# Optimization experiments

Measured on AMD Instinct MI355X. Metric: run time of the kernel, lower is better.

## Reference

```python
import jax, jax.numpy as jnp
import numpy as np

D_MODEL, D_STATE, D_CONV, EXPAND = 1024, 16, 4, 2
D_INNER = EXPAND * D_MODEL
B, L = 2, 2048


def setup_inputs() -> dict:
    key = jax.random.key(0)
    ks = jax.random.split(key, 8)
    s = lambda fan: 1.0 / np.sqrt(fan)
    x = jax.random.normal(ks[0], (B, L, D_MODEL), dtype=jnp.float32)
    W_in = jax.random.normal(ks[1], (2 * D_INNER, D_MODEL), dtype=jnp.float32) * s(D_MODEL)
    conv_w = jax.random.normal(ks[2], (D_INNER, 1, D_CONV), dtype=jnp.float32) * s(D_CONV)
    conv_b = jax.random.normal(ks[3], (D_INNER,), dtype=jnp.float32) * 0.01
    A_log = jnp.log(jnp.abs(jax.random.normal(ks[4], (D_INNER, D_STATE), dtype=jnp.float32)) + 1e-4)
    Dp = jnp.ones((D_INNER,), dtype=jnp.float32)
    W_dt = jax.random.normal(ks[5], (D_INNER, D_INNER), dtype=jnp.float32) * s(D_INNER)
    b_dt = jax.random.normal(ks[6], (D_INNER,), dtype=jnp.float32) * 0.01
    W_out = jax.random.normal(ks[7], (D_MODEL, D_INNER), dtype=jnp.float32) * s(D_INNER)
    return {"x": x, "W_in": W_in, "conv_w": conv_w, "conv_b": conv_b,
            "A_log": A_log, "Dp": Dp, "W_dt": W_dt, "b_dt": b_dt, "W_out": W_out}


def _mamba_fwd(x, W_in, conv_w, conv_b, A_log, Dp, W_dt, b_dt, W_out):
    Bsz, Ln, _ = x.shape
    xz = x @ W_in.T                                  # [B, L, 2*d_inner]
    x_proj, z = jnp.split(xz, 2, axis=-1)            # each [B, L, d_inner]
    # depthwise causal conv1d: left-pad d_conv-1 (matches torch pad + [:L] slice)
    xc = jnp.transpose(x_proj, (0, 2, 1))            # [B, C, L]
    xc = jax.lax.conv_general_dilated(
        xc, conv_w, window_strides=(1,), padding=[(D_CONV - 1, 0)],
        dimension_numbers=("NCH", "OIH", "NCH"), feature_group_count=D_INNER)
    xc = xc + conv_b[None, :, None]
    x_act = jax.nn.silu(jnp.transpose(xc, (0, 2, 1)))  # [B, L, d_inner]
    dt = jax.nn.softplus(x_act @ W_dt.T + b_dt)        # [B, L, d_inner]
    A = -jnp.exp(A_log)                                # [d_inner, d_state]

    def step(h, inp):
        xt, dt_t = inp                                 # [B, d_inner] each
        dA = jnp.exp(dt_t[:, :, None] * A[None])       # [B, d_inner, d_state]
        dB = (dt_t * xt)[:, :, None]                   # broadcast over states
        h = dA * h + dB
        y_t = h.sum(axis=-1) + Dp * xt                 # [B, d_inner]
        return h, y_t

    h0 = jnp.zeros((Bsz, D_INNER, D_STATE), dtype=x.dtype)
    xs = (jnp.transpose(x_act, (1, 0, 2)), jnp.transpose(dt, (1, 0, 2)))  # [L, B, d_inner]
    _, ys = jax.lax.scan(step, h0, xs)
    y_ssm = jnp.transpose(ys, (1, 0, 2))               # [B, L, d_inner]
    y_gated = y_ssm * jax.nn.silu(z)
    return y_gated @ W_out.T                           # [B, L, d_model]


def reference(x, W_in, conv_w, conv_b, A_log, Dp, W_dt, b_dt, W_out):
    return _mamba_fwd(x, W_in, conv_w, conv_b, A_log, Dp, W_dt, b_dt, W_out)
```

## Files before the change

### kernel.cpp

```cpp
#include <hip/hip_runtime.h>

#define DMODEL 1024
#define DSTATE 16
#define DCONV  4
#define DINNER 2048
#define BSZ    2
#define LSEQ   2048
#define MTOT   (BSZ * LSEQ)
#define NCH    64
#define LC     (LSEQ / NCH)
#define LOG2E  1.44269504088896f

typedef unsigned short u16;
typedef __attribute__((ext_vector_type(8))) short short8;
typedef __attribute__((ext_vector_type(8))) unsigned short u16x8;
typedef __attribute__((ext_vector_type(4))) float f32x4;

__device__ __forceinline__ float silu_f(float v) {
  return v * __builtin_amdgcn_rcpf(1.f + __builtin_amdgcn_exp2f(-v * LOG2E));
}

__device__ __forceinline__ u16 f2bf(float f) {
  unsigned int u = __float_as_uint(f);
  u += 0x7FFF + ((u >> 16) & 1);
  return (u16)(u >> 16);
}
__device__ __forceinline__ float bf2f(u16 b) { return __uint_as_float(((unsigned int)b) << 16); }

__device__ __forceinline__ void gload_lds16(const u16* g, u16* l) {
  __builtin_amdgcn_global_load_lds((const __attribute__((address_space(1))) unsigned int*)g,
                                   (__attribute__((address_space(3))) unsigned int*)l, 16, 0, 0);
}

__global__ __launch_bounds__(256)
void cast4(const float4* __restrict__ s0, ushort4* __restrict__ d0, int n0,
           const float4* __restrict__ s1, ushort4* __restrict__ d1, int n1,
           const float4* __restrict__ s2, ushort4* __restrict__ d2, int n2,
           const float4* __restrict__ s3, ushort4* __restrict__ d3, int n3) {
  int i = blockIdx.x * 256 + threadIdx.x;
  const float4* s; ushort4* d;
  if (i < n0)                { s = s0; d = d0; }
  else if ((i -= n0) < n1)   { s = s1; d = d1; }
  else if ((i -= n1) < n2)   { s = s2; d = d2; }
  else if ((i -= n2) < n3)   { s = s3; d = d3; }
  else return;
  float4 v = s[i];
  ushort4 o = { f2bf(v.x), f2bf(v.y), f2bf(v.z), f2bf(v.w) };
  d[i] = o;
}

template<int MODE, int OBF>
__global__ __launch_bounds__(256)
void hgemm64(const u16* __restrict__ A, const u16* __restrict__ B,
             const float* __restrict__ bias, void* __restrict__ Cv,
             int M, int N, int K) {
  __shared__ u16 As[128 * 64];
  __shared__ u16 Bs[128 * 64];
  const int tid  = threadIdx.x;
  const int lane = tid & 63;
  const int w    = tid >> 6;
  const int quad = lane >> 4;
  const int l16  = lane & 15;

  const int nbn = N >> 7, nbm = M >> 7;
  const int pid = blockIdx.x;
  const int npg = 4 * nbn;
  const int fm  = (pid / npg) * 4;
  const int gsz = (nbm - fm < 4) ? (nbm - fm) : 4;
  const int bm  = (fm + (pid % gsz)) << 7;
  const int bn  = ((pid % npg) / gsz) << 7;

  const int wm = (w & 1) * 64;
  const int wn = (w >> 1) * 64;

  const int rseg = lane >> 3;
  const int cd   = (lane & 7) ^ rseg;
  const u16* Ag[4]; const u16* Bg[4]; u16* Al[4]; u16* Bl[4];
#pragma unroll
  for (int s = 0; s < 4; ++s) {
    const int sg = w * 4 + s;
    const int r  = sg * 8 + rseg;
    Ag[s] = A + (size_t)(bm + r) * K + (cd << 3);
    Bg[s] = B + (size_t)(bn + r) * K + (cd << 3);
    Al[s] = &As[sg << 9];
    Bl[s] = &Bs[sg << 9];
  }

  const short8* Afp[4][2];
  const short8* Bfp[4][2];
#pragma unroll
  for (int t = 0; t < 4; ++t) {
    const int ra = wm + 16 * t + l16;
    const int rb = wn + 16 * t + l16;
#pragma unroll
    for (int ks = 0; ks < 2; ++ks) {
      Afp[t][ks] = (const short8*)&As[ra * 64 + (((quad + 4 * ks) ^ (ra & 7)) << 3)];
      Bfp[t][ks] = (const short8*)&Bs[rb * 64 + (((quad + 4 * ks) ^ (rb & 7)) << 3)];
    }
  }

  f32x4 acc[4][4] = {};

  for (int k0 = 0; k0 < K; k0 += 64) {
#pragma unroll
    for (int s = 0; s < 4; ++s) {
      gload_lds16(Ag[s], Al[s]);
      gload_lds16(Bg[s], Bl[s]);
      Ag[s] += 64; Bg[s] += 64;
    }
    __syncthreads();
#pragma unroll
    for (int ks = 0; ks < 2; ++ks) {
      short8 af[4], bf[4];
#pragma unroll
      for (int t = 0; t < 4; ++t) { af[t] = *Afp[t][ks]; bf[t] = *Bfp[t][ks]; }
#pragma unroll
      for (int ti = 0; ti < 4; ++ti)
#pragma unroll
        for (int tj = 0; tj < 4; ++tj)
          acc[ti][tj] = __builtin_amdgcn_mfma_f32_16x16x32_bf16(af[ti], bf[tj],
                                                                acc[ti][tj], 0, 0, 0);
    }
    __syncthreads();
  }

#pragma unroll
  for (int ti = 0; ti < 4; ++ti) {
    const int row0 = bm + wm + 16 * ti + quad * 4;
#pragma unroll
    for (int tj = 0; tj < 4; ++tj) {
      const int col = bn + wn + 16 * tj + l16;
      const float bv = (MODE == 1) ? bias[col] : 0.f;
#pragma unroll
      for (int i = 0; i < 4; ++i) {
        float v = acc[ti][tj][i] + bv;
        if (MODE == 1) v = (v > 20.f) ? v : __logf(1.f + __expf(v));
        if (OBF) ((u16*)Cv)[(size_t)(row0 + i) * N + col] = f2bf(v);
        else     ((float*)Cv)[(size_t)(row0 + i) * N + col] = v;
      }
    }
  }
}

__global__ __launch_bounds__(256)
void conv_silu(const u16* __restrict__ xz, const float* __restrict__ conv_w,
               const float* __restrict__ conv_b, u16* __restrict__ xact) {
  const int i = blockIdx.x * 256 + threadIdx.x;
  const int ko = i & 255;
  const int t  = (i >> 8) & (LSEQ - 1);
  const int b  = i >> 19;
  const int c  = ko << 3;
  float a[8];
  float4 w[8];
#pragma unroll
  for (int j = 0; j < 8; ++j) {
    a[j] = conv_b[c + j];
    w[j] = *(const float4*)(conv_w + (c + j) * DCONV);
  }
#pragma unroll
  for (int k = 0; k < DCONV; ++k) {
    const int tt = t + k - (DCONV - 1);
    if (tt >= 0) {
      const u16x8 v = *(const u16x8*)(xz + ((size_t)(b * LSEQ + tt) << 12) + c);
#pragma unroll
      for (int j = 0; j < 8; ++j)
        a[j] = fmaf(bf2f(v[j]), ((const float*)&w[j])[k], a[j]);
    }
  }
  u16x8 o;
#pragma unroll
  for (int j = 0; j < 8; ++j) o[j] = f2bf(silu_f(a[j]));
  *(u16x8*)(xact + ((size_t)(b * LSEQ + t) << 11) + c) = o;
}


__global__ __launch_bounds__(256, 2)
void scan_pass1(const u16* __restrict__ dtb, const u16* __restrict__ xact,
                const float* __restrict__ A_log,
                float* __restrict__ hbuf, float* __restrict__ sumdt) {
  const int gid = blockIdx.x * 256 + threadIdx.x;
  const int c  = gid & (DINNER - 1);
  const int ch = (gid >> 11) & (NCH - 1);
  const int b  = gid >> 17;
  float a2[16];
#pragma unroll
  for (int s = 0; s < 16; ++s)
    a2[s] = -__expf(A_log[c * DSTATE + s]) * LOG2E;
  const size_t base = ((size_t)(b * LSEQ + ch * LC) << 11) + c;
  float h[16] = {};
  float sd = 0.f;
  for (int j = 0; j < LC; j += 2) {
    const float dt0 = bf2f(dtb [base + ((size_t)j << 11)]);
    const float xv0 = bf2f(xact[base + ((size_t)j << 11)]);
    const float dt1 = bf2f(dtb [base + ((size_t)(j + 1) << 11)]);
    const float xv1 = bf2f(xact[base + ((size_t)(j + 1) << 11)]);
    const float dx0 = dt0 * xv0, dx1 = dt1 * xv1;
    sd += dt0 + dt1;
#pragma unroll
    for (int s = 0; s < 16; ++s)
      h[s] = fmaf(__builtin_amdgcn_exp2f(dt0 * a2[s]), h[s], dx0);
#pragma unroll
    for (int s = 0; s < 16; ++s)
      h[s] = fmaf(__builtin_amdgcn_exp2f(dt1 * a2[s]), h[s], dx1);
  }
  float4* ho = (float4*)&hbuf[(((size_t)(b * NCH + ch) * DINNER) + c) << 4];
#pragma unroll
  for (int q = 0; q < 4; ++q) {
    float4 v = { h[4 * q], h[4 * q + 1], h[4 * q + 2], h[4 * q + 3] };
    ho[q] = v;
  }
  sumdt[(size_t)(b * NCH + ch) * DINNER + c] = sd;
}

__global__ __launch_bounds__(256)
void scan_combine(float* __restrict__ hbuf, const float* __restrict__ sumdt,
                  const float* __restrict__ A_log) {
  const int gid = blockIdx.x * 256 + threadIdx.x;
  const int s = gid & 15;
  const int c = (gid >> 4) & (DINNER - 1);
  const int b = gid >> 15;
  const float a2 = -__expf(A_log[c * DSTATE + s]) * LOG2E;
  float h = 0.f;
  for (int k = 0; k < NCH; ++k) {
    const size_t o = (((size_t)(b * NCH + k) * DINNER) + c) * 16 + s;
    const float he = hbuf[o];
    const float sd = sumdt[(size_t)(b * NCH + k) * DINNER + c];
    hbuf[o] = h;
    h = fmaf(__builtin_amdgcn_exp2f(sd * a2), h, he);
  }
}

__global__ __launch_bounds__(256, 2)
void scan_pass3(const u16* __restrict__ dtb, const u16* __restrict__ xact,
                const u16* __restrict__ xz, const float* __restrict__ A_log,
                const float* __restrict__ Dp, const float* __restrict__ hbuf,
                u16* __restrict__ yg) {
  const int gid = blockIdx.x * 256 + threadIdx.x;
  const int c  = gid & (DINNER - 1);
  const int ch = (gid >> 11) & (NCH - 1);
  const int b  = gid >> 17;
  float a2[16];
#pragma unroll
  for (int s = 0; s < 16; ++s)
    a2[s] = -__expf(A_log[c * DSTATE + s]) * LOG2E;
  const float dp = Dp[c];
  float h[16];
  const float4* hi = (const float4*)&hbuf[(((size_t)(b * NCH + ch) * DINNER) + c) << 4];
#pragma unroll
  for (int q = 0; q < 4; ++q) {
    float4 v = hi[q];
    h[4 * q] = v.x; h[4 * q + 1] = v.y; h[4 * q + 2] = v.z; h[4 * q + 3] = v.w;
  }
  const size_t base  = ((size_t)(b * LSEQ + ch * LC) << 11) + c;
  const size_t zbase = ((size_t)(b * LSEQ + ch * LC) << 12) + DINNER + c;
  for (int j = 0; j < LC; j += 2) {
    const float dt0 = bf2f(dtb [base + ((size_t)j << 11)]);
    const float xv0 = bf2f(xact[base + ((size_t)j << 11)]);
    const float zv0 = bf2f(xz[zbase + ((size_t)j << 12)]);
    const float dt1 = bf2f(dtb [base + ((size_t)(j + 1) << 11)]);
    const float xv1 = bf2f(xact[base + ((size_t)(j + 1) << 11)]);
    const float zv1 = bf2f(xz[zbase + ((size_t)(j + 1) << 12)]);
    const float dx0 = dt0 * xv0, dx1 = dt1 * xv1;
    float y0 = 0.f, y1 = 0.f;
#pragma unroll
    for (int s = 0; s < 16; ++s) {
      h[s] = fmaf(__builtin_amdgcn_exp2f(dt0 * a2[s]), h[s], dx0);
      y0 += h[s];
    }
#pragma unroll
    for (int s = 0; s < 16; ++s) {
      h[s] = fmaf(__builtin_amdgcn_exp2f(dt1 * a2[s]), h[s], dx1);
      y1 += h[s];
    }
    y0 = fmaf(dp, xv0, y0);
    y1 = fmaf(dp, xv1, y1);
    yg[base + ((size_t)j << 11)]       = f2bf(y0 * silu_f(zv0));
    yg[base + ((size_t)(j + 1) << 11)] = f2bf(y1 * silu_f(zv1));
  }
}

extern "C" void kernel_launch(void* const* d_in, const int* in_sizes, int n_in,
                              void* d_out, int out_size, void* d_ws, size_t ws_size,
                              hipStream_t stream) {
  const float* x      = (const float*)d_in[0];
  const float* W_in   = (const float*)d_in[1];
  const float* conv_w = (const float*)d_in[2];
  const float* conv_b = (const float*)d_in[3];
  const float* A_log  = (const float*)d_in[4];
  const float* Dp     = (const float*)d_in[5];
  const float* W_dt   = (const float*)d_in[6];
  const float* b_dt   = (const float*)d_in[7];
  const float* W_out  = (const float*)d_in[8];
  float* out = (float*)d_out;

  float* ws    = (float*)d_ws;
  float* hbuf  = ws;
  float* sumdt = hbuf + (size_t)BSZ * NCH * DINNER * 16;
  u16* xz   = (u16*)(sumdt + (size_t)BSZ * NCH * DINNER);
  u16* dtb  = xz   + (size_t)MTOT * 2 * DINNER;
  u16* xbf  = dtb  + (size_t)MTOT * DINNER;
  u16* wibf = xbf  + (size_t)MTOT * DMODEL;
  u16* wdbf = wibf + (size_t)2 * DINNER * DMODEL;
  u16* wobf = wdbf + (size_t)DINNER * DINNER;
  u16* xact = wobf + (size_t)DMODEL * DINNER;
  u16* yg   = xact + (size_t)MTOT * DINNER;

  const dim3 blk(256);

  const int n0 = MTOT * DMODEL / 4, n1 = 2 * DINNER * DMODEL / 4;
  const int n2 = DINNER * DINNER / 4, n3 = DMODEL * DINNER / 4;
  cast4<<<(n0 + n1 + n2 + n3) / 256, blk, 0, stream>>>(
      (const float4*)x, (ushort4*)xbf, n0,
      (const float4*)W_in, (ushort4*)wibf, n1,
      (const float4*)W_dt, (ushort4*)wdbf, n2,
      (const float4*)W_out, (ushort4*)wobf, n3);

  hgemm64<0, 1><<<(MTOT / 128) * (2 * DINNER / 128), blk, 0, stream>>>(
      xbf, wibf, nullptr, xz, MTOT, 2 * DINNER, DMODEL);
  conv_silu<<<(MTOT * 256) / 256, blk, 0, stream>>>(xz, conv_w, conv_b, xact);
  hgemm64<1, 1><<<(MTOT / 128) * (DINNER / 128), blk, 0, stream>>>(
      xact, wdbf, b_dt, dtb, MTOT, DINNER, DINNER);
  scan_pass1<<<BSZ * NCH * DINNER / 256, blk, 0, stream>>>(dtb, xact, A_log, hbuf, sumdt);
  scan_combine<<<BSZ * DINNER * 16 / 256, blk, 0, stream>>>(hbuf, sumdt, A_log);
  scan_pass3<<<BSZ * NCH * DINNER / 256, blk, 0, stream>>>(dtb, xact, xz, A_log, Dp, hbuf, yg);
  hgemm64<0, 0><<<(MTOT / 128) * (DMODEL / 128), blk, 0, stream>>>(
      yg, wobf, nullptr, out, MTOT, DMODEL, DINNER);
}
```

Measured before the change: 336.7 us.

## Fuse chunked scan into one LDS-staged kernel and add narrow-N output GEMM

Replaces the three-kernel chunked scan (pass1, combine, pass3) with a single kernel per 4 channels. That kernel stages dt and x for the whole sequence in LDS, runs a 64-chunk Hillis-Steele prefix combine in shared memory, and writes gated outputs coalesced. This removes the global hbuf/sumdt round trips and two launches. It also adds a 128x64-tile GEMM for the output projection so N=1024 yields more blocks. The risks are the large LDS footprint, which limits the scan to one block per CU with only 512*2 blocks, and many barriers in the tree combine.

```diff
diff --git a/kernel.cpp b/kernel.cpp
--- a/kernel.cpp
+++ b/kernel.cpp
@@ -143,6 +143,98 @@
 }
 
 __global__ __launch_bounds__(256)
+void hgemm_n64(const u16* __restrict__ A, const u16* __restrict__ B,
+               float* __restrict__ C, int M, int N, int K) {
+  __shared__ u16 As[128 * 64];
+  __shared__ u16 Bs[64 * 64];
+  const int tid  = threadIdx.x;
+  const int lane = tid & 63;
+  const int w    = tid >> 6;
+  const int quad = lane >> 4;
+  const int l16  = lane & 15;
+
+  const int nbn = N >> 6, nbm = M >> 7;
+  const int pid = blockIdx.x;
+  const int npg = 4 * nbn;
+  const int fm  = (pid / npg) * 4;
+  const int gsz = (nbm - fm < 4) ? (nbm - fm) : 4;
+  const int bm  = (fm + (pid % gsz)) << 7;
+  const int bn  = ((pid % npg) / gsz) << 6;
+
+  const int wm = (w & 1) * 64;
+  const int wn = (w >> 1) * 32;
+
+  const int rseg = lane >> 3;
+  const int cd   = (lane & 7) ^ rseg;
+  const u16* Gp[6]; u16* Lp[6];
+#pragma unroll
+  for (int q = 0; q < 6; ++q) {
+    const int g = w * 6 + q;
+    if (g < 16) {
+      const int r = g * 8 + rseg;
+      Gp[q] = A + (size_t)(bm + r) * K + (cd << 3);
+      Lp[q] = &As[g << 9];
+    } else {
+      const int r = (g - 16) * 8 + rseg;
+      Gp[q] = B + (size_t)(bn + r) * K + (cd << 3);
+      Lp[q] = &Bs[(g - 16) << 9];
+    }
+  }
+
+  const short8* Afp[4][2];
+  const short8* Bfp[2][2];
+#pragma unroll
+  for (int t = 0; t < 4; ++t) {
+    const int ra = wm + 16 * t + l16;
+#pragma unroll
+    for (int ks = 0; ks < 2; ++ks)
+      Afp[t][ks] = (const short8*)&As[ra * 64 + (((quad + 4 * ks) ^ (ra & 7)) << 3)];
+  }
+#pragma unroll
+  for (int t = 0; t < 2; ++t) {
+    const int rb = wn + 16 * t + l16;
+#pragma unroll
+    for (int ks = 0; ks < 2; ++ks)
+      Bfp[t][ks] = (const short8*)&Bs[rb * 64 + (((quad + 4 * ks) ^ (rb & 7)) << 3)];
+  }
+
+  f32x4 acc[4][2] = {};
+
+  for (int k0 = 0; k0 < K; k0 += 64) {
+#pragma unroll
+    for (int q = 0; q < 6; ++q) { gload_lds16(Gp[q], Lp[q]); Gp[q] += 64; }
+    __syncthreads();
+#pragma unroll
+    for (int ks = 0; ks < 2; ++ks) {
+      short8 af[4], bf[2];
+#pragma unroll
+      for (int t = 0; t < 4; ++t) af[t] = *Afp[t][ks];
+#pragma unroll
+      for (int t = 0; t < 2; ++t) bf[t] = *Bfp[t][ks];
+#pragma unroll
+      for (int ti = 0; ti < 4; ++ti)
+#pragma unroll
+        for (int tj = 0; tj < 2; ++tj)
+          acc[ti][tj] = __builtin_amdgcn_mfma_f32_16x16x32_bf16(af[ti], bf[tj],
+                                                                acc[ti][tj], 0, 0, 0);
+    }
+    __syncthreads();
+  }
+
+#pragma unroll
+  for (int ti = 0; ti < 4; ++ti) {
+    const int row0 = bm + wm + 16 * ti + quad * 4;
+#pragma unroll
+    for (int tj = 0; tj < 2; ++tj) {
+      const int col = bn + wn + 16 * tj + l16;
+#pragma unroll
+      for (int i = 0; i < 4; ++i)
+        C[(size_t)(row0 + i) * N + col] = acc[ti][tj][i];
+    }
+  }
+}
+
+__global__ __launch_bounds__(256)
 void conv_silu(const u16* __restrict__ xz, const float* __restrict__ conv_w,
                const float* __restrict__ conv_b, u16* __restrict__ xact) {
   const int i = blockIdx.x * 256 + threadIdx.x;
@@ -173,93 +265,95 @@
   *(u16x8*)(xact + ((size_t)(b * LSEQ + t) << 11) + c) = o;
 }
 
-
-__global__ __launch_bounds__(256, 2)
-void scan_pass1(const u16* __restrict__ dtb, const u16* __restrict__ xact,
-                const float* __restrict__ A_log,
-                float* __restrict__ hbuf, float* __restrict__ sumdt) {
-  const int gid = blockIdx.x * 256 + threadIdx.x;
-  const int c  = gid & (DINNER - 1);
-  const int ch = (gid >> 11) & (NCH - 1);
-  const int b  = gid >> 17;
-  float a2[16];
-#pragma unroll
-  for (int s = 0; s < 16; ++s)
-    a2[s] = -__expf(A_log[c * DSTATE + s]) * LOG2E;
-  const size_t base = ((size_t)(b * LSEQ + ch * LC) << 11) + c;
-  float h[16] = {};
-  float sd = 0.f;
-  for (int j = 0; j < LC; j += 2) {
-    const float dt0 = bf2f(dtb [base + ((size_t)j << 11)]);
-    const float xv0 = bf2f(xact[base + ((size_t)j << 11)]);
-    const float dt1 = bf2f(dtb [base + ((size_t)(j + 1) << 11)]);
-    const float xv1 = bf2f(xact[base + ((size_t)(j + 1) << 11)]);
-    const float dx0 = dt0 * xv0, dx1 = dt1 * xv1;
-    sd += dt0 + dt1;
-#pragma unroll
-    for (int s = 0; s < 16; ++s)
-      h[s] = fmaf(__builtin_amdgcn_exp2f(dt0 * a2[s]), h[s], dx0);
-#pragma unroll
-    for (int s = 0; s < 16; ++s)
-      h[s] = fmaf(__builtin_amdgcn_exp2f(dt1 * a2[s]), h[s], dx1);
-  }
-  float4* ho = (float4*)&hbuf[(((size_t)(b * NCH + ch) * DINNER) + c) << 4];
-#pragma unroll
-  for (int q = 0; q < 4; ++q) {
-    float4 v = { h[4 * q], h[4 * q + 1], h[4 * q + 2], h[4 * q + 3] };
-    ho[q] = v;
-  }
-  sumdt[(size_t)(b * NCH + ch) * DINNER + c] = sd;
+__device__ __forceinline__ int swiz(int t, int ch) {
+  return (t * 4 + ch) ^ (((t >> 5) & 7) << 2);
 }
 
 __global__ __launch_bounds__(256)
-void scan_combine(float* __restrict__ hbuf, const float* __restrict__ sumdt,
-                  const float* __restrict__ A_log) {
-  const int gid = blockIdx.x * 256 + threadIdx.x;
-  const int s = gid & 15;
-  const int c = (gid >> 4) & (DINNER - 1);
-  const int b = gid >> 15;
-  const float a2 = -__expf(A_log[c * DSTATE + s]) * LOG2E;
-  float h = 0.f;
-  for (int k = 0; k < NCH; ++k) {
-    const size_t o = (((size_t)(b * NCH + k) * DINNER) + c) * 16 + s;
-    const float he = hbuf[o];
-    const float sd = sumdt[(size_t)(b * NCH + k) * DINNER + c];
-    hbuf[o] = h;
-    h = fmaf(__builtin_amdgcn_exp2f(sd * a2), h, he);
-  }
-}
-
-__global__ __launch_bounds__(256, 2)
-void scan_pass3(const u16* __restrict__ dtb, const u16* __restrict__ xact,
+void scan_fused(const u16* __restrict__ dtb, const u16* __restrict__ xact,
                 const u16* __restrict__ xz, const float* __restrict__ A_log,
-                const float* __restrict__ Dp, const float* __restrict__ hbuf,
-                u16* __restrict__ yg) {
-  const int gid = blockIdx.x * 256 + threadIdx.x;
-  const int c  = gid & (DINNER - 1);
-  const int ch = (gid >> 11) & (NCH - 1);
-  const int b  = gid >> 17;
+                const float* __restrict__ Dp, u16* __restrict__ yg) {
+  __shared__ unsigned int stage[LSEQ * 4];
+  __shared__ float tree[256 * 17];
+  const int tid = threadIdx.x;
+  const int ch  = tid & 3;
+  const int ck  = tid >> 2;
+  const int b   = blockIdx.x >> 9;
+  const int c   = ((blockIdx.x & 511) << 2) + ch;
+
+#pragma unroll 4
+  for (int i = 0; i < 32; ++i) {
+    const int t = i * 64 + ck;
+    const size_t g = ((size_t)(b * LSEQ + t) << 11) + c;
+    stage[swiz(t, ch)] = ((unsigned int)xact[g] << 16) | (unsigned int)dtb[g];
+  }
   float a2[16];
 #pragma unroll
   for (int s = 0; s < 16; ++s)
     a2[s] = -__expf(A_log[c * DSTATE + s]) * LOG2E;
   const float dp = Dp[c];
-  float h[16];
-  const float4* hi = (const float4*)&hbuf[(((size_t)(b * NCH + ch) * DINNER) + c) << 4];
-#pragma unroll
-  for (int q = 0; q < 4; ++q) {
-    float4 v = hi[q];
-    h[4 * q] = v.x; h[4 * q + 1] = v.y; h[4 * q + 2] = v.z; h[4 * q + 3] = v.w;
-  }
-  const size_t base  = ((size_t)(b * LSEQ + ch * LC) << 11) + c;
-  const size_t zbase = ((size_t)(b * LSEQ + ch * LC) << 12) + DINNER + c;
+  __syncthreads();
+
+  float h[16] = {};
+  float sd = 0.f;
+  const int t0 = ck * LC;
   for (int j = 0; j < LC; j += 2) {
-    const float dt0 = bf2f(dtb [base + ((size_t)j << 11)]);
-    const float xv0 = bf2f(xact[base + ((size_t)j << 11)]);
-    const float zv0 = bf2f(xz[zbase + ((size_t)j << 12)]);
-    const float dt1 = bf2f(dtb [base + ((size_t)(j + 1) << 11)]);
-    const float xv1 = bf2f(xact[base + ((size_t)(j + 1) << 11)]);
-    const float zv1 = bf2f(xz[zbase + ((size_t)(j + 1) << 12)]);
+    const unsigned int w0 = stage[swiz(t0 + j, ch)];
+    const unsigned int w1 = stage[swiz(t0 + j + 1, ch)];
+    const float dt0 = bf2f((u16)w0), xv0 = bf2f((u16)(w0 >> 16));
+    const float dt1 = bf2f((u16)w1), xv1 = bf2f((u16)(w1 >> 16));
+    const float dx0 = dt0 * xv0, dx1 = dt1 * xv1;
+    sd += dt0 + dt1;
+#pragma unroll
+    for (int s = 0; s < 16; ++s)
+      h[s] = fmaf(__builtin_amdgcn_exp2f(dt0 * a2[s]), h[s], dx0);
+#pragma unroll
+    for (int s = 0; s < 16; ++s)
+      h[s] = fmaf(__builtin_amdgcn_exp2f(dt1 * a2[s]), h[s], dx1);
+  }
+
+  float* ent = &tree[tid * 17];
+  ent[0] = sd;
+#pragma unroll
+  for (int s = 0; s < 16; ++s) ent[1 + s] = h[s];
+#pragma unroll
+  for (int off = 1; off < 64; off <<= 1) {
+    __syncthreads();
+    float psd = 0.f, ph[16];
+    const bool has = (ck >= off);
+    if (has) {
+      const float* p = &tree[(tid - 4 * off) * 17];
+      psd = p[0];
+#pragma unroll
+      for (int s = 0; s < 16; ++s) ph[s] = p[1 + s];
+    }
+    __syncthreads();
+    if (has) {
+#pragma unroll
+      for (int s = 0; s < 16; ++s)
+        h[s] = fmaf(__builtin_amdgcn_exp2f(sd * a2[s]), ph[s], h[s]);
+      sd += psd;
+      ent[0] = sd;
+#pragma unroll
+      for (int s = 0; s < 16; ++s) ent[1 + s] = h[s];
+    }
+  }
+  __syncthreads();
+
+  if (ck == 0) {
+#pragma unroll
+    for (int s = 0; s < 16; ++s) h[s] = 0.f;
+  } else {
+    const float* p = &tree[(tid - 4) * 17];
+#pragma unroll
+    for (int s = 0; s < 16; ++s) h[s] = p[1 + s];
+  }
+
+  for (int j = 0; j < LC; j += 2) {
+    const unsigned int w0 = stage[swiz(t0 + j, ch)];
+    const unsigned int w1 = stage[swiz(t0 + j + 1, ch)];
+    const float dt0 = bf2f((u16)w0), xv0 = bf2f((u16)(w0 >> 16));
+    const float dt1 = bf2f((u16)w1), xv1 = bf2f((u16)(w1 >> 16));
     const float dx0 = dt0 * xv0, dx1 = dt1 * xv1;
     float y0 = 0.f, y1 = 0.f;
 #pragma unroll
@@ -272,10 +366,17 @@
       h[s] = fmaf(__builtin_amdgcn_exp2f(dt1 * a2[s]), h[s], dx1);
       y1 += h[s];
     }
-    y0 = fmaf(dp, xv0, y0);
-    y1 = fmaf(dp, xv1, y1);
-    yg[base + ((size_t)j << 11)]       = f2bf(y0 * silu_f(zv0));
-    yg[base + ((size_t)(j + 1) << 11)] = f2bf(y1 * silu_f(zv1));
+    stage[swiz(t0 + j, ch)]     = (unsigned int)f2bf(fmaf(dp, xv0, y0));
+    stage[swiz(t0 + j + 1, ch)] = (unsigned int)f2bf(fmaf(dp, xv1, y1));
+  }
+  __syncthreads();
+
+#pragma unroll 4
+  for (int i = 0; i < 32; ++i) {
+    const int t = i * 64 + ck;
+    const float y  = bf2f((u16)stage[swiz(t, ch)]);
+    const float zv = bf2f(xz[((size_t)(b * LSEQ + t) << 12) + DINNER + c]);
+    yg[((size_t)(b * LSEQ + t) << 11) + c] = f2bf(y * silu_f(zv));
   }
 }
 
@@ -293,10 +394,7 @@
   const float* W_out  = (const float*)d_in[8];
   float* out = (float*)d_out;
 
-  float* ws    = (float*)d_ws;
-  float* hbuf  = ws;
-  float* sumdt = hbuf + (size_t)BSZ * NCH * DINNER * 16;
-  u16* xz   = (u16*)(sumdt + (size_t)BSZ * NCH * DINNER);
+  u16* xz   = (u16*)d_ws;
   u16* dtb  = xz   + (size_t)MTOT * 2 * DINNER;
   u16* xbf  = dtb  + (size_t)MTOT * DINNER;
   u16* wibf = xbf  + (size_t)MTOT * DMODEL;
@@ -320,9 +418,7 @@
   conv_silu<<<(MTOT * 256) / 256, blk, 0, stream>>>(xz, conv_w, conv_b, xact);
   hgemm64<1, 1><<<(MTOT / 128) * (DINNER / 128), blk, 0, stream>>>(
       xact, wdbf, b_dt, dtb, MTOT, DINNER, DINNER);
-  scan_pass1<<<BSZ * NCH * DINNER / 256, blk, 0, stream>>>(dtb, xact, A_log, hbuf, sumdt);
-  scan_combine<<<BSZ * DINNER * 16 / 256, blk, 0, stream>>>(hbuf, sumdt, A_log);
-  scan_pass3<<<BSZ * NCH * DINNER / 256, blk, 0, stream>>>(dtb, xact, xz, A_log, Dp, hbuf, yg);
-  hgemm64<0, 0><<<(MTOT / 128) * (DMODEL / 128), blk, 0, stream>>>(
-      yg, wobf, nullptr, out, MTOT, DMODEL, DINNER);
-}
+  scan_fused<<<BSZ * (DINNER / 4), blk, 0, stream>>>(dtb, xact, xz, A_log, Dp, yg);
+  hgemm_n64<<<(MTOT / 128) * (DMODEL / 64), blk, 0, stream>>>(
+      yg, wobf, out, MTOT, DMODEL, DINNER);
+}
```

After: 353.5 us. 1.05x slower.
